# Optimization experiments

Hardware: AMD Instinct MI355X
Metric: run time of the kernel (lower is better)

Reference implementation:

```python
import jax, jax.numpy as jnp
import numpy as np

N_NODES = 50000
N_EDGES = 600000
D_IN = 128
D_OUT = 128


def setup_inputs() -> dict:
    key = jax.random.key(0)
    k1, k2, k3, k4, k5 = jax.random.split(key, 5)
    x = jax.random.normal(k1, (N_NODES, D_IN), dtype=jnp.float32)
    src = jax.random.randint(k2, (N_EDGES,), 0, N_NODES, dtype=jnp.int64)
    # guarantee every node has at least one incoming edge so in_degree >= 1
    # (DGL graphs in this repo use self-loop-augmented graphs; sqrt(deg) must be > 0)
    dst_rand = jax.random.randint(k3, (N_EDGES - N_NODES,), 0, N_NODES, dtype=jnp.int64)
    dst = jnp.concatenate([jnp.arange(N_NODES, dtype=jnp.int64), dst_rand])
    W = jax.random.normal(k4, (D_IN, D_OUT), dtype=jnp.float32) * (1.0 / np.sqrt(D_IN))
    b = jax.random.normal(k5, (D_OUT,), dtype=jnp.float32) * 0.02
    return {"x": x, "src": src, "dst": dst, "W": W, "b": b}


def reference(x, src, dst, W, b):
    # in-degrees (graph.in_degrees()): count of edges pointing at each node
    ones = jnp.ones_like(dst, dtype=jnp.float32)
    in_deg = jax.ops.segment_sum(ones, dst, num_segments=N_NODES)  # [N]
    # per-edge normalization: 1 / sqrt(deg_src * deg_dst)
    norm = jax.lax.rsqrt(in_deg[src] * in_deg[dst])  # [E]
    # gather src features, normalize, edge-wise matmul with W, add bias per edge
    msg = (x[src] * norm[:, None]) @ W + b  # [E, D_OUT]
    # sum-scatter messages to destination nodes (dgl.function.sum)
    out = jax.ops.segment_sum(msg, dst, num_segments=N_NODES)  # [N, D_OUT]
    return out
```

## Files before the change

kernel.cpp:

```cpp
#include <hip/hip_runtime.h>

#define N_NODES 50000
#define N_EDGES 600000
#define DIM 128
#define CAP 64

static __device__ __forceinline__ int idx_is32(const void* idxbuf) {
  return ((const int*)idxbuf)[1] != 0;
}
static __device__ __forceinline__ int load_idx(const void* p, int i, int is32) {
  return is32 ? ((const int*)p)[i] : (int)((const long long*)p)[i];
}
static __device__ __forceinline__ unsigned bf16_2(float a, float b) {
  unsigned ua = __float_as_uint(a), ub = __float_as_uint(b);
  ua = (ua + 0x7fffu + ((ua >> 16) & 1u)) >> 16;
  ub = (ub + 0x7fffu + ((ub >> 16) & 1u)) >> 16;
  return ua | (ub << 16);
}

__global__ void build_k(const void* __restrict__ src, const void* __restrict__ dst,
                        int* __restrict__ cursor, unsigned short* __restrict__ sorted) {
  const int half = N_EDGES / 2;
  int e0 = blockIdx.x * blockDim.x + threadIdx.x;
  if (e0 >= half) return;
  int is32 = idx_is32(dst);
#pragma unroll
  for (int h = 0; h < 2; ++h) {
    int e = e0 + h * half;
    int d = load_idx(dst, e, is32);
    int s = load_idx(src, e, is32);
    int p = atomicAdd(&cursor[d], 1);
    if (p < CAP) sorted[(d << 6) + p] = (unsigned short)s;
  }
}

__launch_bounds__(256, 3)
__global__ void ygemm_k(const float* __restrict__ x, const float4* __restrict__ W4,
                        const int* __restrict__ deg, unsigned* __restrict__ yb) {
  __shared__ float As[32 * 132];
  __shared__ float Ws[32 * 128];
  int t = threadIdx.x;
  int n0 = blockIdx.x * 128;
  int ng = t & 15, cg = t >> 4;

  float acc[8][8];
#pragma unroll
  for (int ii = 0; ii < 8; ++ii)
#pragma unroll
    for (int jj = 0; jj < 8; ++jj) acc[ii][jj] = 0.f;

  for (int s = 0; s < 4; ++s) {
    float4* Ws4 = (float4*)Ws;
#pragma unroll
    for (int i = 0; i < 4; ++i)
      Ws4[t + i * 256] = W4[s * 32 * 32 + t + i * 256];
#pragma unroll
    for (int i = 0; i < 4; ++i) {
      int idx = t + i * 256;
      int r = idx >> 3, q = idx & 7;
      int n = n0 + r;
      float4 v = make_float4(0.f, 0.f, 0.f, 0.f);
      if (n < N_NODES) v = ((const float4*)x)[n * 32 + s * 8 + q];
      As[(q * 4 + 0) * 132 + r] = v.x;
      As[(q * 4 + 1) * 132 + r] = v.y;
      As[(q * 4 + 2) * 132 + r] = v.z;
      As[(q * 4 + 3) * 132 + r] = v.w;
    }
    __syncthreads();
#pragma unroll 2
    for (int k = 0; k < 32; ++k) {
      float4 a0 = *(const float4*)&As[k * 132 + ng * 4];
      float4 a1 = *(const float4*)&As[k * 132 + 64 + ng * 4];
      float4 w0 = *(const float4*)&Ws[k * 128 + cg * 4];
      float4 w1 = *(const float4*)&Ws[k * 128 + 64 + cg * 4];
      float a[8] = {a0.x, a0.y, a0.z, a0.w, a1.x, a1.y, a1.z, a1.w};
      float w[8] = {w0.x, w0.y, w0.z, w0.w, w1.x, w1.y, w1.z, w1.w};
#pragma unroll
      for (int ii = 0; ii < 8; ++ii)
#pragma unroll
        for (int jj = 0; jj < 8; ++jj) acc[ii][jj] += a[ii] * w[jj];
    }
    __syncthreads();
  }

#pragma unroll
  for (int ii = 0; ii < 8; ++ii) {
    int n = n0 + (ii >> 2) * 64 + ng * 4 + (ii & 3);
    if (n < N_NODES) {
      float rs = rsqrtf((float)deg[n]);
      uint2 u0, u1;
      u0.x = bf16_2(acc[ii][0] * rs, acc[ii][1] * rs);
      u0.y = bf16_2(acc[ii][2] * rs, acc[ii][3] * rs);
      u1.x = bf16_2(acc[ii][4] * rs, acc[ii][5] * rs);
      u1.y = bf16_2(acc[ii][6] * rs, acc[ii][7] * rs);
      *(uint2*)&yb[(long)n * 64 + cg * 2] = u0;
      *(uint2*)&yb[(long)n * 64 + 32 + cg * 2] = u1;
    }
  }
}

__launch_bounds__(256)
__global__ void agg_k(const unsigned* __restrict__ yb,
                      const unsigned short* __restrict__ sorted,
                      const int* __restrict__ deg, const float2* __restrict__ b2,
                      float2* __restrict__ out2) {
  long gid = (long)blockIdx.x * blockDim.x + threadIdx.x;
  int d = (int)(gid >> 6);
  int lane = (int)gid & 63;
  if (d >= N_NODES) return;
  int base = d << 6;
  int dg = deg[d];
  int cnt = min(dg, CAP);
  float ax0 = 0, ax1 = 0, ax2 = 0, ax3 = 0;
  float ay0 = 0, ay1 = 0, ay2 = 0, ay3 = 0;
  int i = 0;
  for (; i + 3 < cnt; i += 4) {
    uint2 sp = *(const uint2*)&sorted[base + i];
    int s0 = sp.x & 0xffff, s1 = sp.x >> 16;
    int s2 = sp.y & 0xffff, s3 = sp.y >> 16;
    unsigned u0 = yb[s0 * 64 + lane], u1 = yb[s1 * 64 + lane];
    unsigned u2 = yb[s2 * 64 + lane], u3 = yb[s3 * 64 + lane];
    ax0 += __uint_as_float(u0 << 16);
    ay0 += __uint_as_float(u0 & 0xffff0000u);
    ax1 += __uint_as_float(u1 << 16);
    ay1 += __uint_as_float(u1 & 0xffff0000u);
    ax2 += __uint_as_float(u2 << 16);
    ay2 += __uint_as_float(u2 & 0xffff0000u);
    ax3 += __uint_as_float(u3 << 16);
    ay3 += __uint_as_float(u3 & 0xffff0000u);
  }
  for (; i < cnt; ++i) {
    int s = sorted[base + i];
    unsigned u = yb[s * 64 + lane];
    ax0 += __uint_as_float(u << 16);
    ay0 += __uint_as_float(u & 0xffff0000u);
  }
  float rd = rsqrtf((float)dg);
  float fd = (float)dg;
  float2 bv = b2[lane];
  float2 r;
  r.x = rd * ((ax0 + ax1) + (ax2 + ax3)) + fd * bv.x;
  r.y = rd * ((ay0 + ay1) + (ay2 + ay3)) + fd * bv.y;
  out2[(long)d * 64 + lane] = r;
}

__global__ void hist_k(const void* __restrict__ dst, int* __restrict__ deg) {
  int e = blockIdx.x * blockDim.x + threadIdx.x;
  if (e >= N_EDGES) return;
  atomicAdd(&deg[load_idx(dst, e, idx_is32(dst))], 1);
}
__global__ void scatter4_k(const float4* __restrict__ x4, const void* __restrict__ src,
                           const void* __restrict__ dst, const int* __restrict__ deg,
                           float* out) {
  long gid = (long)blockIdx.x * blockDim.x + threadIdx.x;
  long e = gid >> 5;
  int lane = (int)gid & 31;
  if (e >= N_EDGES) return;
  int is32 = idx_is32(dst);
  int s = load_idx(src, (int)e, is32);
  int d = load_idx(dst, (int)e, is32);
  float nrm = rsqrtf((float)deg[s] * (float)deg[d]);
  float4 v = x4[(long)s * 32 + lane];
  float* o = out + (long)d * DIM + lane * 4;
  unsafeAtomicAdd(o + 0, v.x * nrm);
  unsafeAtomicAdd(o + 1, v.y * nrm);
  unsafeAtomicAdd(o + 2, v.z * nrm);
  unsafeAtomicAdd(o + 3, v.w * nrm);
}
__launch_bounds__(256, 3)
__global__ void gemm2_k(const float* __restrict__ agg, const float4* __restrict__ W4,
                        const float* __restrict__ b, const int* __restrict__ degi,
                        float* __restrict__ out) {
  __shared__ float As[32 * 132];
  __shared__ float Ws[32 * 128];
  int t = threadIdx.x;
  int n0 = blockIdx.x * 128;
  int ng = t & 15, cg = t >> 4;
  float acc[8][8];
#pragma unroll
  for (int ii = 0; ii < 8; ++ii)
#pragma unroll
    for (int jj = 0; jj < 8; ++jj) acc[ii][jj] = 0.f;
  for (int s = 0; s < 4; ++s) {
    float4* Ws4 = (float4*)Ws;
#pragma unroll
    for (int i = 0; i < 4; ++i)
      Ws4[t + i * 256] = W4[s * 32 * 32 + t + i * 256];
#pragma unroll
    for (int i = 0; i < 4; ++i) {
      int idx = t + i * 256;
      int r = idx >> 3, q = idx & 7;
      int n = n0 + r;
      float4 v = make_float4(0.f, 0.f, 0.f, 0.f);
      if (n < N_NODES) v = ((const float4*)agg)[n * 32 + s * 8 + q];
      As[(q * 4 + 0) * 132 + r] = v.x;
      As[(q * 4 + 1) * 132 + r] = v.y;
      As[(q * 4 + 2) * 132 + r] = v.z;
      As[(q * 4 + 3) * 132 + r] = v.w;
    }
    __syncthreads();
#pragma unroll 2
    for (int k = 0; k < 32; ++k) {
      float4 a0 = *(const float4*)&As[k * 132 + ng * 4];
      float4 a1 = *(const float4*)&As[k * 132 + 64 + ng * 4];
      float4 w0 = *(const float4*)&Ws[k * 128 + cg * 4];
      float4 w1 = *(const float4*)&Ws[k * 128 + 64 + cg * 4];
      float a[8] = {a0.x, a0.y, a0.z, a0.w, a1.x, a1.y, a1.z, a1.w};
      float w[8] = {w0.x, w0.y, w0.z, w0.w, w1.x, w1.y, w1.z, w1.w};
#pragma unroll
      for (int ii = 0; ii < 8; ++ii)
#pragma unroll
        for (int jj = 0; jj < 8; ++jj) acc[ii][jj] += a[ii] * w[jj];
    }
    __syncthreads();
  }
  float4 bv0 = ((const float4*)b)[cg];
  float4 bv1 = ((const float4*)b)[16 + cg];
#pragma unroll
  for (int ii = 0; ii < 8; ++ii) {
    int n = n0 + (ii >> 2) * 64 + ng * 4 + (ii & 3);
    if (n < N_NODES) {
      float dg = (float)degi[n];
      float4 o0, o1;
      o0.x = acc[ii][0] + dg * bv0.x; o0.y = acc[ii][1] + dg * bv0.y;
      o0.z = acc[ii][2] + dg * bv0.z; o0.w = acc[ii][3] + dg * bv0.w;
      o1.x = acc[ii][4] + dg * bv1.x; o1.y = acc[ii][5] + dg * bv1.y;
      o1.z = acc[ii][6] + dg * bv1.z; o1.w = acc[ii][7] + dg * bv1.w;
      *(float4*)&out[(long)n * 128 + cg * 4] = o0;
      *(float4*)&out[(long)n * 128 + 64 + cg * 4] = o1;
    }
  }
}

static inline size_t al(size_t x) { return (x + 255) & ~(size_t)255; }

extern "C" void kernel_launch(void* const* d_in, const int* in_sizes, int n_in,
                              void* d_out, int out_size, void* d_ws, size_t ws_size,
                              hipStream_t stream) {
  const float* x = (const float*)d_in[0];
  const void* src = d_in[1];
  const void* dst = d_in[2];
  const float* W = (const float*)d_in[3];
  const float* b = (const float*)d_in[4];
  float* out = (float*)d_out;
  char* ws = (char*)d_ws;

  size_t o_sorted = al((size_t)N_NODES * 4);
  size_t o_yb = al(o_sorted + (size_t)N_NODES * CAP * 2);
  size_t need = o_yb + (size_t)N_NODES * DIM * 2;

  int* cursor = (int*)ws;
  unsigned short* sorted = (unsigned short*)(ws + o_sorted);
  unsigned* yb = (unsigned*)(ws + o_yb);

  if (ws_size >= need) {
    hipMemsetAsync(cursor, 0, (size_t)N_NODES * 4, stream);
    build_k<<<(N_EDGES / 2 + 255) / 256, 256, 0, stream>>>(src, dst, cursor, sorted);
    ygemm_k<<<(N_NODES + 127) / 128, 256, 0, stream>>>(x, (const float4*)W, cursor, yb);
    agg_k<<<(N_NODES * 64 + 255) / 256, 256, 0, stream>>>(
        yb, sorted, cursor, (const float2*)b, (float2*)out);
  } else {
    hipMemsetAsync(cursor, 0, (size_t)N_NODES * 4, stream);
    hipMemsetAsync(out, 0, (size_t)N_NODES * DIM * 4, stream);
    hist_k<<<(N_EDGES + 255) / 256, 256, 0, stream>>>(dst, cursor);
    scatter4_k<<<((long)N_EDGES * 32 + 255) / 256, 256, 0, stream>>>(
        (const float4*)x, src, dst, cursor, out);
    gemm2_k<<<(N_NODES + 127) / 128, 256, 0, stream>>>(out, (const float4*)W, b,
                                                       cursor, out);
  }
}
```

Baseline: 174.3 us.

## Fuse build, GEMM and aggregation into one cooperative persistent kernel

Replaces the memset plus three kernel launches with a single cooperative kernel that separates the cursor clear, edge bucketing, per-node GEMM and gather-aggregation phases with grid-wide syncs. The aim is to remove launch overhead and inter-kernel gaps. The aggregation loop is also unrolled to 8 gathers per iteration for more memory-level parallelism. The trade-offs are a fixed 512-block grid capped at 2 blocks per SM by launch bounds, grid.sync costs, and a fallback to the old path if the cooperative launch fails.

```diff
diff --git a/kernel.cpp b/kernel.cpp
--- a/kernel.cpp
+++ b/kernel.cpp
@@ -1,9 +1,14 @@
 #include <hip/hip_runtime.h>
+#include <hip/hip_cooperative_groups.h>
+
+namespace cg = cooperative_groups;
 
 #define N_NODES 50000
 #define N_EDGES 600000
 #define DIM 128
 #define CAP 64
+#define GRID_BLKS 512
+#define NT ((N_NODES + 127) / 128)
 
 static __device__ __forceinline__ int idx_is32(const void* idxbuf) {
   return ((const int*)idxbuf)[1] != 0;
@@ -16,6 +21,151 @@
   ua = (ua + 0x7fffu + ((ua >> 16) & 1u)) >> 16;
   ub = (ub + 0x7fffu + ((ub >> 16) & 1u)) >> 16;
   return ua | (ub << 16);
+}
+
+__global__ __launch_bounds__(256, 2) void fused_k(
+    const float* __restrict__ x, const void* __restrict__ src,
+    const void* __restrict__ dst, const float4* __restrict__ W4,
+    const float2* __restrict__ b2, int* __restrict__ cursor,
+    unsigned short* __restrict__ sorted, unsigned* __restrict__ yb,
+    float2* __restrict__ out2) {
+  cg::grid_group grid = cg::this_grid();
+  __shared__ float As[32 * 132];
+  __shared__ float Ws[32 * 128];
+  int t = threadIdx.x;
+  int bid = blockIdx.x;
+  int gtid = bid * 256 + t;
+
+  for (int i = gtid; i < N_NODES; i += GRID_BLKS * 256) cursor[i] = 0;
+  grid.sync();
+
+  {
+    int is32 = idx_is32(dst);
+    for (int e = gtid; e < N_EDGES; e += GRID_BLKS * 256) {
+      int d = load_idx(dst, e, is32);
+      int s = load_idx(src, e, is32);
+      int p = atomicAdd(&cursor[d], 1);
+      if (p < CAP) sorted[(d << 6) + p] = (unsigned short)s;
+    }
+  }
+  grid.sync();
+
+  for (int tile = bid; tile < NT; tile += GRID_BLKS) {
+    int n0 = tile * 128;
+    int ng = t & 15, cg_ = t >> 4;
+    float acc[8][8];
+#pragma unroll
+    for (int ii = 0; ii < 8; ++ii)
+#pragma unroll
+      for (int jj = 0; jj < 8; ++jj) acc[ii][jj] = 0.f;
+
+    for (int s = 0; s < 4; ++s) {
+      float4* Ws4 = (float4*)Ws;
+#pragma unroll
+      for (int i = 0; i < 4; ++i)
+        Ws4[t + i * 256] = W4[s * 32 * 32 + t + i * 256];
+#pragma unroll
+      for (int i = 0; i < 4; ++i) {
+        int idx = t + i * 256;
+        int r = idx >> 3, q = idx & 7;
+        int n = n0 + r;
+        float4 v = make_float4(0.f, 0.f, 0.f, 0.f);
+        if (n < N_NODES) v = ((const float4*)x)[n * 32 + s * 8 + q];
+        As[(q * 4 + 0) * 132 + r] = v.x;
+        As[(q * 4 + 1) * 132 + r] = v.y;
+        As[(q * 4 + 2) * 132 + r] = v.z;
+        As[(q * 4 + 3) * 132 + r] = v.w;
+      }
+      __syncthreads();
+#pragma unroll 2
+      for (int k = 0; k < 32; ++k) {
+        float4 a0 = *(const float4*)&As[k * 132 + ng * 4];
+        float4 a1 = *(const float4*)&As[k * 132 + 64 + ng * 4];
+        float4 w0 = *(const float4*)&Ws[k * 128 + cg_ * 4];
+        float4 w1 = *(const float4*)&Ws[k * 128 + 64 + cg_ * 4];
+        float a[8] = {a0.x, a0.y, a0.z, a0.w, a1.x, a1.y, a1.z, a1.w};
+        float w[8] = {w0.x, w0.y, w0.z, w0.w, w1.x, w1.y, w1.z, w1.w};
+#pragma unroll
+        for (int ii = 0; ii < 8; ++ii)
+#pragma unroll
+          for (int jj = 0; jj < 8; ++jj) acc[ii][jj] += a[ii] * w[jj];
+      }
+      __syncthreads();
+    }
+#pragma unroll
+    for (int ii = 0; ii < 8; ++ii) {
+      int n = n0 + (ii >> 2) * 64 + ng * 4 + (ii & 3);
+      if (n < N_NODES) {
+        float rs = rsqrtf((float)cursor[n]);
+        uint2 u0, u1;
+        u0.x = bf16_2(acc[ii][0] * rs, acc[ii][1] * rs);
+        u0.y = bf16_2(acc[ii][2] * rs, acc[ii][3] * rs);
+        u1.x = bf16_2(acc[ii][4] * rs, acc[ii][5] * rs);
+        u1.y = bf16_2(acc[ii][6] * rs, acc[ii][7] * rs);
+        *(uint2*)&yb[(long)n * 64 + cg_ * 2] = u0;
+        *(uint2*)&yb[(long)n * 64 + 32 + cg_ * 2] = u1;
+      }
+    }
+  }
+  grid.sync();
+
+  {
+    int lane = gtid & 63;
+    int w0 = gtid >> 6;
+    const int nwaves = GRID_BLKS * 256 / 64;
+    for (int d = w0; d < N_NODES; d += nwaves) {
+      int base = d << 6;
+      int dg = cursor[d];
+      int cnt = min(dg, CAP);
+      float ax0 = 0, ax1 = 0, ax2 = 0, ax3 = 0, ax4 = 0, ax5 = 0, ax6 = 0, ax7 = 0;
+      float ay0 = 0, ay1 = 0, ay2 = 0, ay3 = 0, ay4 = 0, ay5 = 0, ay6 = 0, ay7 = 0;
+      int i = 0;
+      for (; i + 7 < cnt; i += 8) {
+        uint4 sp = *(const uint4*)&sorted[base + i];
+        int s0 = sp.x & 0xffff, s1 = sp.x >> 16;
+        int s2 = sp.y & 0xffff, s3 = sp.y >> 16;
+        int s4 = sp.z & 0xffff, s5 = sp.z >> 16;
+        int s6 = sp.w & 0xffff, s7 = sp.w >> 16;
+        unsigned u0 = yb[s0 * 64 + lane], u1 = yb[s1 * 64 + lane];
+        unsigned u2 = yb[s2 * 64 + lane], u3 = yb[s3 * 64 + lane];
+        unsigned u4 = yb[s4 * 64 + lane], u5 = yb[s5 * 64 + lane];
+        unsigned u6 = yb[s6 * 64 + lane], u7 = yb[s7 * 64 + lane];
+        ax0 += __uint_as_float(u0 << 16); ay0 += __uint_as_float(u0 & 0xffff0000u);
+        ax1 += __uint_as_float(u1 << 16); ay1 += __uint_as_float(u1 & 0xffff0000u);
+        ax2 += __uint_as_float(u2 << 16); ay2 += __uint_as_float(u2 & 0xffff0000u);
+        ax3 += __uint_as_float(u3 << 16); ay3 += __uint_as_float(u3 & 0xffff0000u);
+        ax4 += __uint_as_float(u4 << 16); ay4 += __uint_as_float(u4 & 0xffff0000u);
+        ax5 += __uint_as_float(u5 << 16); ay5 += __uint_as_float(u5 & 0xffff0000u);
+        ax6 += __uint_as_float(u6 << 16); ay6 += __uint_as_float(u6 & 0xffff0000u);
+        ax7 += __uint_as_float(u7 << 16); ay7 += __uint_as_float(u7 & 0xffff0000u);
+      }
+      if (i + 3 < cnt) {
+        uint2 sp = *(const uint2*)&sorted[base + i];
+        int s0 = sp.x & 0xffff, s1 = sp.x >> 16;
+        int s2 = sp.y & 0xffff, s3 = sp.y >> 16;
+        unsigned u0 = yb[s0 * 64 + lane], u1 = yb[s1 * 64 + lane];
+        unsigned u2 = yb[s2 * 64 + lane], u3 = yb[s3 * 64 + lane];
+        ax0 += __uint_as_float(u0 << 16); ay0 += __uint_as_float(u0 & 0xffff0000u);
+        ax1 += __uint_as_float(u1 << 16); ay1 += __uint_as_float(u1 & 0xffff0000u);
+        ax2 += __uint_as_float(u2 << 16); ay2 += __uint_as_float(u2 & 0xffff0000u);
+        ax3 += __uint_as_float(u3 << 16); ay3 += __uint_as_float(u3 & 0xffff0000u);
+        i += 4;
+      }
+      for (; i < cnt; ++i) {
+        int s = sorted[base + i];
+        unsigned u = yb[s * 64 + lane];
+        ax0 += __uint_as_float(u << 16);
+        ay0 += __uint_as_float(u & 0xffff0000u);
+      }
+      float rd = rsqrtf((float)dg);
+      float fd = (float)dg;
+      float2 bv = b2[lane];
+      float2 r;
+      r.x = rd * (((ax0 + ax1) + (ax2 + ax3)) + ((ax4 + ax5) + (ax6 + ax7))) + fd * bv.x;
+      r.y = rd * (((ay0 + ay1) + (ay2 + ay3)) + ((ay4 + ay5) + (ay6 + ay7))) + fd * bv.y;
+      out2[(long)d * 64 + lane] = r;
+    }
+  }
 }
 
 __global__ void build_k(const void* __restrict__ src, const void* __restrict__ dst,
@@ -41,14 +191,12 @@
   __shared__ float Ws[32 * 128];
   int t = threadIdx.x;
   int n0 = blockIdx.x * 128;
-  int ng = t & 15, cg = t >> 4;
-
+  int ng = t & 15, cg_ = t >> 4;
   float acc[8][8];
 #pragma unroll
   for (int ii = 0; ii < 8; ++ii)
 #pragma unroll
     for (int jj = 0; jj < 8; ++jj) acc[ii][jj] = 0.f;
-
   for (int s = 0; s < 4; ++s) {
     float4* Ws4 = (float4*)Ws;
 #pragma unroll
@@ -71,8 +219,8 @@
     for (int k = 0; k < 32; ++k) {
       float4 a0 = *(const float4*)&As[k * 132 + ng * 4];
       float4 a1 = *(const float4*)&As[k * 132 + 64 + ng * 4];
-      float4 w0 = *(const float4*)&Ws[k * 128 + cg * 4];
-      float4 w1 = *(const float4*)&Ws[k * 128 + 64 + cg * 4];
+      float4 w0 = *(const float4*)&Ws[k * 128 + cg_ * 4];
+      float4 w1 = *(const float4*)&Ws[k * 128 + 64 + cg_ * 4];
       float a[8] = {a0.x, a0.y, a0.z, a0.w, a1.x, a1.y, a1.z, a1.w};
       float w[8] = {w0.x, w0.y, w0.z, w0.w, w1.x, w1.y, w1.z, w1.w};
 #pragma unroll
@@ -82,7 +230,6 @@
     }
     __syncthreads();
   }
-
 #pragma unroll
   for (int ii = 0; ii < 8; ++ii) {
     int n = n0 + (ii >> 2) * 64 + ng * 4 + (ii & 3);
@@ -93,8 +240,8 @@
       u0.y = bf16_2(acc[ii][2] * rs, acc[ii][3] * rs);
       u1.x = bf16_2(acc[ii][4] * rs, acc[ii][5] * rs);
       u1.y = bf16_2(acc[ii][6] * rs, acc[ii][7] * rs);
-      *(uint2*)&yb[(long)n * 64 + cg * 2] = u0;
-      *(uint2*)&yb[(long)n * 64 + 32 + cg * 2] = u1;
+      *(uint2*)&yb[(long)n * 64 + cg_ * 2] = u0;
+      *(uint2*)&yb[(long)n * 64 + 32 + cg_ * 2] = u1;
     }
   }
 }
@@ -120,14 +267,10 @@
     int s2 = sp.y & 0xffff, s3 = sp.y >> 16;
     unsigned u0 = yb[s0 * 64 + lane], u1 = yb[s1 * 64 + lane];
     unsigned u2 = yb[s2 * 64 + lane], u3 = yb[s3 * 64 + lane];
-    ax0 += __uint_as_float(u0 << 16);
-    ay0 += __uint_as_float(u0 & 0xffff0000u);
-    ax1 += __uint_as_float(u1 << 16);
-    ay1 += __uint_as_float(u1 & 0xffff0000u);
-    ax2 += __uint_as_float(u2 << 16);
-    ay2 += __uint_as_float(u2 & 0xffff0000u);
-    ax3 += __uint_as_float(u3 << 16);
-    ay3 += __uint_as_float(u3 & 0xffff0000u);
+    ax0 += __uint_as_float(u0 << 16); ay0 += __uint_as_float(u0 & 0xffff0000u);
+    ax1 += __uint_as_float(u1 << 16); ay1 += __uint_as_float(u1 & 0xffff0000u);
+    ax2 += __uint_as_float(u2 << 16); ay2 += __uint_as_float(u2 & 0xffff0000u);
+    ax3 += __uint_as_float(u3 << 16); ay3 += __uint_as_float(u3 & 0xffff0000u);
   }
   for (; i < cnt; ++i) {
     int s = sorted[base + i];
@@ -175,7 +318,7 @@
   __shared__ float Ws[32 * 128];
   int t = threadIdx.x;
   int n0 = blockIdx.x * 128;
-  int ng = t & 15, cg = t >> 4;
+  int ng = t & 15, cg_ = t >> 4;
   float acc[8][8];
 #pragma unroll
   for (int ii = 0; ii < 8; ++ii)
@@ -203,8 +346,8 @@
     for (int k = 0; k < 32; ++k) {
       float4 a0 = *(const float4*)&As[k * 132 + ng * 4];
       float4 a1 = *(const float4*)&As[k * 132 + 64 + ng * 4];
-      float4 w0 = *(const float4*)&Ws[k * 128 + cg * 4];
-      float4 w1 = *(const float4*)&Ws[k * 128 + 64 + cg * 4];
+      float4 w0 = *(const float4*)&Ws[k * 128 + cg_ * 4];
+      float4 w1 = *(const float4*)&Ws[k * 128 + 64 + cg_ * 4];
       float a[8] = {a0.x, a0.y, a0.z, a0.w, a1.x, a1.y, a1.z, a1.w};
       float w[8] = {w0.x, w0.y, w0.z, w0.w, w1.x, w1.y, w1.z, w1.w};
 #pragma unroll
@@ -214,8 +357,8 @@
     }
     __syncthreads();
   }
-  float4 bv0 = ((const float4*)b)[cg];
-  float4 bv1 = ((const float4*)b)[16 + cg];
+  float4 bv0 = ((const float4*)b)[cg_];
+  float4 bv1 = ((const float4*)b)[16 + cg_];
 #pragma unroll
   for (int ii = 0; ii < 8; ++ii) {
     int n = n0 + (ii >> 2) * 64 + ng * 4 + (ii & 3);
@@ -226,8 +369,8 @@
       o0.z = acc[ii][2] + dg * bv0.z; o0.w = acc[ii][3] + dg * bv0.w;
       o1.x = acc[ii][4] + dg * bv1.x; o1.y = acc[ii][5] + dg * bv1.y;
       o1.z = acc[ii][6] + dg * bv1.z; o1.w = acc[ii][7] + dg * bv1.w;
-      *(float4*)&out[(long)n * 128 + cg * 4] = o0;
-      *(float4*)&out[(long)n * 128 + 64 + cg * 4] = o1;
+      *(float4*)&out[(long)n * 128 + cg_ * 4] = o0;
+      *(float4*)&out[(long)n * 128 + 64 + cg_ * 4] = o1;
     }
   }
 }
@@ -254,11 +397,21 @@
   unsigned* yb = (unsigned*)(ws + o_yb);
 
   if (ws_size >= need) {
-    hipMemsetAsync(cursor, 0, (size_t)N_NODES * 4, stream);
-    build_k<<<(N_EDGES / 2 + 255) / 256, 256, 0, stream>>>(src, dst, cursor, sorted);
-    ygemm_k<<<(N_NODES + 127) / 128, 256, 0, stream>>>(x, (const float4*)W, cursor, yb);
-    agg_k<<<(N_NODES * 64 + 255) / 256, 256, 0, stream>>>(
-        yb, sorted, cursor, (const float2*)b, (float2*)out);
+    const float4* W4 = (const float4*)W;
+    const float2* b2 = (const float2*)b;
+    float2* out2 = (float2*)out;
+    void* kargs[] = {(void*)&x,      (void*)&src,  (void*)&dst,
+                     (void*)&W4,     (void*)&b2,   (void*)&cursor,
+                     (void*)&sorted, (void*)&yb,   (void*)&out2};
+    hipError_t err = hipLaunchCooperativeKernel(
+        (const void*)fused_k, dim3(GRID_BLKS), dim3(256), kargs, 0, stream);
+    if (err != hipSuccess) {
+      hipMemsetAsync(cursor, 0, (size_t)N_NODES * 4, stream);
+      build_k<<<(N_EDGES / 2 + 255) / 256, 256, 0, stream>>>(src, dst, cursor, sorted);
+      ygemm_k<<<(N_NODES + 127) / 128, 256, 0, stream>>>(x, (const float4*)W, cursor, yb);
+      agg_k<<<(N_NODES * 64 + 255) / 256, 256, 0, stream>>>(
+          yb, sorted, cursor, (const float2*)b, (float2*)out);
+    }
   } else {
     hipMemsetAsync(cursor, 0, (size_t)N_NODES * 4, stream);
     hipMemsetAsync(out, 0, (size_t)N_NODES * DIM * 4, stream);
```

New measurement: 387.4 us. +122.3%, slower.

## Fold cursor zeroing into GEMM, move src-degree norm into aggregation, widen unroll

Applied to the files above, without the earlier changes.

The GEMM now runs first and zeroes the degree cursor itself, which removes the separate memset launch. The GEMM no longer depends on degrees, so it can precede the graph build. The per-source rsqrt(deg) scaling moves from the GEMM epilogue into the aggregation kernel, which adds a gathered deg load and an rsqrt per edge. The aggregation loop is unrolled to 8 edges with more independent accumulators for extra memory-level parallelism. The cost is more random loads in agg_k and higher register use.

```diff
diff --git a/kernel.cpp b/kernel.cpp
--- a/kernel.cpp
+++ b/kernel.cpp
@@ -18,31 +18,18 @@
   return ua | (ub << 16);
 }
 
-__global__ void build_k(const void* __restrict__ src, const void* __restrict__ dst,
-                        int* __restrict__ cursor, unsigned short* __restrict__ sorted) {
-  const int half = N_EDGES / 2;
-  int e0 = blockIdx.x * blockDim.x + threadIdx.x;
-  if (e0 >= half) return;
-  int is32 = idx_is32(dst);
-#pragma unroll
-  for (int h = 0; h < 2; ++h) {
-    int e = e0 + h * half;
-    int d = load_idx(dst, e, is32);
-    int s = load_idx(src, e, is32);
-    int p = atomicAdd(&cursor[d], 1);
-    if (p < CAP) sorted[(d << 6) + p] = (unsigned short)s;
-  }
-}
-
 __launch_bounds__(256, 3)
 __global__ void ygemm_k(const float* __restrict__ x, const float4* __restrict__ W4,
-                        const int* __restrict__ deg, unsigned* __restrict__ yb) {
+                        int* __restrict__ cursor, unsigned* __restrict__ yb) {
   __shared__ float As[32 * 132];
   __shared__ float Ws[32 * 128];
   int t = threadIdx.x;
   int n0 = blockIdx.x * 128;
-  int ng = t & 15, cg = t >> 4;
-
+  {
+    int z = blockIdx.x * 256 + t;
+    if (z < N_NODES) cursor[z] = 0;
+  }
+  int ng = t & 15, cg_ = t >> 4;
   float acc[8][8];
 #pragma unroll
   for (int ii = 0; ii < 8; ++ii)
@@ -71,8 +58,8 @@
     for (int k = 0; k < 32; ++k) {
       float4 a0 = *(const float4*)&As[k * 132 + ng * 4];
       float4 a1 = *(const float4*)&As[k * 132 + 64 + ng * 4];
-      float4 w0 = *(const float4*)&Ws[k * 128 + cg * 4];
-      float4 w1 = *(const float4*)&Ws[k * 128 + 64 + cg * 4];
+      float4 w0 = *(const float4*)&Ws[k * 128 + cg_ * 4];
+      float4 w1 = *(const float4*)&Ws[k * 128 + 64 + cg_ * 4];
       float a[8] = {a0.x, a0.y, a0.z, a0.w, a1.x, a1.y, a1.z, a1.w};
       float w[8] = {w0.x, w0.y, w0.z, w0.w, w1.x, w1.y, w1.z, w1.w};
 #pragma unroll
@@ -82,20 +69,34 @@
     }
     __syncthreads();
   }
-
 #pragma unroll
   for (int ii = 0; ii < 8; ++ii) {
     int n = n0 + (ii >> 2) * 64 + ng * 4 + (ii & 3);
     if (n < N_NODES) {
-      float rs = rsqrtf((float)deg[n]);
       uint2 u0, u1;
-      u0.x = bf16_2(acc[ii][0] * rs, acc[ii][1] * rs);
-      u0.y = bf16_2(acc[ii][2] * rs, acc[ii][3] * rs);
-      u1.x = bf16_2(acc[ii][4] * rs, acc[ii][5] * rs);
-      u1.y = bf16_2(acc[ii][6] * rs, acc[ii][7] * rs);
-      *(uint2*)&yb[(long)n * 64 + cg * 2] = u0;
-      *(uint2*)&yb[(long)n * 64 + 32 + cg * 2] = u1;
-    }
+      u0.x = bf16_2(acc[ii][0], acc[ii][1]);
+      u0.y = bf16_2(acc[ii][2], acc[ii][3]);
+      u1.x = bf16_2(acc[ii][4], acc[ii][5]);
+      u1.y = bf16_2(acc[ii][6], acc[ii][7]);
+      *(uint2*)&yb[(long)n * 64 + cg_ * 2] = u0;
+      *(uint2*)&yb[(long)n * 64 + 32 + cg_ * 2] = u1;
+    }
+  }
+}
+
+__global__ void build_k(const void* __restrict__ src, const void* __restrict__ dst,
+                        int* __restrict__ cursor, unsigned short* __restrict__ sorted) {
+  const int half = N_EDGES / 2;
+  int e0 = blockIdx.x * blockDim.x + threadIdx.x;
+  if (e0 >= half) return;
+  int is32 = idx_is32(dst);
+#pragma unroll
+  for (int h = 0; h < 2; ++h) {
+    int e = e0 + h * half;
+    int d = load_idx(dst, e, is32);
+    int s = load_idx(src, e, is32);
+    int p = atomicAdd(&cursor[d], 1);
+    if (p < CAP) sorted[(d << 6) + p] = (unsigned short)s;
   }
 }
 
@@ -111,36 +112,59 @@
   int base = d << 6;
   int dg = deg[d];
   int cnt = min(dg, CAP);
-  float ax0 = 0, ax1 = 0, ax2 = 0, ax3 = 0;
-  float ay0 = 0, ay1 = 0, ay2 = 0, ay3 = 0;
+  float ax0 = 0, ax1 = 0, ax2 = 0, ax3 = 0, ax4 = 0, ax5 = 0, ax6 = 0, ax7 = 0;
+  float ay0 = 0, ay1 = 0, ay2 = 0, ay3 = 0, ay4 = 0, ay5 = 0, ay6 = 0, ay7 = 0;
   int i = 0;
-  for (; i + 3 < cnt; i += 4) {
+  for (; i + 7 < cnt; i += 8) {
+    uint4 sp = *(const uint4*)&sorted[base + i];
+    int s0 = sp.x & 0xffff, s1 = sp.x >> 16;
+    int s2 = sp.y & 0xffff, s3 = sp.y >> 16;
+    int s4 = sp.z & 0xffff, s5 = sp.z >> 16;
+    int s6 = sp.w & 0xffff, s7 = sp.w >> 16;
+    float n0 = rsqrtf((float)deg[s0]), n1 = rsqrtf((float)deg[s1]);
+    float n2 = rsqrtf((float)deg[s2]), n3 = rsqrtf((float)deg[s3]);
+    float n4 = rsqrtf((float)deg[s4]), n5 = rsqrtf((float)deg[s5]);
+    float n6 = rsqrtf((float)deg[s6]), n7 = rsqrtf((float)deg[s7]);
+    unsigned u0 = yb[s0 * 64 + lane], u1 = yb[s1 * 64 + lane];
+    unsigned u2 = yb[s2 * 64 + lane], u3 = yb[s3 * 64 + lane];
+    unsigned u4 = yb[s4 * 64 + lane], u5 = yb[s5 * 64 + lane];
+    unsigned u6 = yb[s6 * 64 + lane], u7 = yb[s7 * 64 + lane];
+    ax0 += n0 * __uint_as_float(u0 << 16); ay0 += n0 * __uint_as_float(u0 & 0xffff0000u);
+    ax1 += n1 * __uint_as_float(u1 << 16); ay1 += n1 * __uint_as_float(u1 & 0xffff0000u);
+    ax2 += n2 * __uint_as_float(u2 << 16); ay2 += n2 * __uint_as_float(u2 & 0xffff0000u);
+    ax3 += n3 * __uint_as_float(u3 << 16); ay3 += n3 * __uint_as_float(u3 & 0xffff0000u);
+    ax4 += n4 * __uint_as_float(u4 << 16); ay4 += n4 * __uint_as_float(u4 & 0xffff0000u);
+    ax5 += n5 * __uint_as_float(u5 << 16); ay5 += n5 * __uint_as_float(u5 & 0xffff0000u);
+    ax6 += n6 * __uint_as_float(u6 << 16); ay6 += n6 * __uint_as_float(u6 & 0xffff0000u);
+    ax7 += n7 * __uint_as_float(u7 << 16); ay7 += n7 * __uint_as_float(u7 & 0xffff0000u);
+  }
+  if (i + 3 < cnt) {
     uint2 sp = *(const uint2*)&sorted[base + i];
     int s0 = sp.x & 0xffff, s1 = sp.x >> 16;
     int s2 = sp.y & 0xffff, s3 = sp.y >> 16;
+    float n0 = rsqrtf((float)deg[s0]), n1 = rsqrtf((float)deg[s1]);
+    float n2 = rsqrtf((float)deg[s2]), n3 = rsqrtf((float)deg[s3]);
     unsigned u0 = yb[s0 * 64 + lane], u1 = yb[s1 * 64 + lane];
     unsigned u2 = yb[s2 * 64 + lane], u3 = yb[s3 * 64 + lane];
-    ax0 += __uint_as_float(u0 << 16);
-    ay0 += __uint_as_float(u0 & 0xffff0000u);
-    ax1 += __uint_as_float(u1 << 16);
-    ay1 += __uint_as_float(u1 & 0xffff0000u);
-    ax2 += __uint_as_float(u2 << 16);
-    ay2 += __uint_as_float(u2 & 0xffff0000u);
-    ax3 += __uint_as_float(u3 << 16);
-    ay3 += __uint_as_float(u3 & 0xffff0000u);
+    ax0 += n0 * __uint_as_float(u0 << 16); ay0 += n0 * __uint_as_float(u0 & 0xffff0000u);
+    ax1 += n1 * __uint_as_float(u1 << 16); ay1 += n1 * __uint_as_float(u1 & 0xffff0000u);
+    ax2 += n2 * __uint_as_float(u2 << 16); ay2 += n2 * __uint_as_float(u2 & 0xffff0000u);
+    ax3 += n3 * __uint_as_float(u3 << 16); ay3 += n3 * __uint_as_float(u3 & 0xffff0000u);
+    i += 4;
   }
   for (; i < cnt; ++i) {
     int s = sorted[base + i];
+    float n = rsqrtf((float)deg[s]);
     unsigned u = yb[s * 64 + lane];
-    ax0 += __uint_as_float(u << 16);
-    ay0 += __uint_as_float(u & 0xffff0000u);
+    ax0 += n * __uint_as_float(u << 16);
+    ay0 += n * __uint_as_float(u & 0xffff0000u);
   }
   float rd = rsqrtf((float)dg);
   float fd = (float)dg;
   float2 bv = b2[lane];
   float2 r;
-  r.x = rd * ((ax0 + ax1) + (ax2 + ax3)) + fd * bv.x;
-  r.y = rd * ((ay0 + ay1) + (ay2 + ay3)) + fd * bv.y;
+  r.x = rd * (((ax0 + ax1) + (ax2 + ax3)) + ((ax4 + ax5) + (ax6 + ax7))) + fd * bv.x;
+  r.y = rd * (((ay0 + ay1) + (ay2 + ay3)) + ((ay4 + ay5) + (ay6 + ay7))) + fd * bv.y;
   out2[(long)d * 64 + lane] = r;
 }
 
@@ -175,7 +199,7 @@
   __shared__ float Ws[32 * 128];
   int t = threadIdx.x;
   int n0 = blockIdx.x * 128;
-  int ng = t & 15, cg = t >> 4;
+  int ng = t & 15, cg_ = t >> 4;
   float acc[8][8];
 #pragma unroll
   for (int ii = 0; ii < 8; ++ii)
@@ -203,8 +227,8 @@
     for (int k = 0; k < 32; ++k) {
       float4 a0 = *(const float4*)&As[k * 132 + ng * 4];
       float4 a1 = *(const float4*)&As[k * 132 + 64 + ng * 4];
-      float4 w0 = *(const float4*)&Ws[k * 128 + cg * 4];
-      float4 w1 = *(const float4*)&Ws[k * 128 + 64 + cg * 4];
+      float4 w0 = *(const float4*)&Ws[k * 128 + cg_ * 4];
+      float4 w1 = *(const float4*)&Ws[k * 128 + 64 + cg_ * 4];
       float a[8] = {a0.x, a0.y, a0.z, a0.w, a1.x, a1.y, a1.z, a1.w};
       float w[8] = {w0.x, w0.y, w0.z, w0.w, w1.x, w1.y, w1.z, w1.w};
 #pragma unroll
@@ -214,8 +238,8 @@
     }
     __syncthreads();
   }
-  float4 bv0 = ((const float4*)b)[cg];
-  float4 bv1 = ((const float4*)b)[16 + cg];
+  float4 bv0 = ((const float4*)b)[cg_];
+  float4 bv1 = ((const float4*)b)[16 + cg_];
 #pragma unroll
   for (int ii = 0; ii < 8; ++ii) {
     int n = n0 + (ii >> 2) * 64 + ng * 4 + (ii & 3);
@@ -226,8 +250,8 @@
       o0.z = acc[ii][2] + dg * bv0.z; o0.w = acc[ii][3] + dg * bv0.w;
       o1.x = acc[ii][4] + dg * bv1.x; o1.y = acc[ii][5] + dg * bv1.y;
       o1.z = acc[ii][6] + dg * bv1.z; o1.w = acc[ii][7] + dg * bv1.w;
-      *(float4*)&out[(long)n * 128 + cg * 4] = o0;
-      *(float4*)&out[(long)n * 128 + 64 + cg * 4] = o1;
+      *(float4*)&out[(long)n * 128 + cg_ * 4] = o0;
+      *(float4*)&out[(long)n * 128 + 64 + cg_ * 4] = o1;
     }
   }
 }
@@ -254,9 +278,8 @@
   unsigned* yb = (unsigned*)(ws + o_yb);
 
   if (ws_size >= need) {
-    hipMemsetAsync(cursor, 0, (size_t)N_NODES * 4, stream);
+    ygemm_k<<<(N_NODES + 127) / 128, 256, 0, stream>>>(x, (const float4*)W, cursor, yb);
     build_k<<<(N_EDGES / 2 + 255) / 256, 256, 0, stream>>>(src, dst, cursor, sorted);
-    ygemm_k<<<(N_NODES + 127) / 128, 256, 0, stream>>>(x, (const float4*)W, cursor, yb);
     agg_k<<<(N_NODES * 64 + 255) / 256, 256, 0, stream>>>(
         yb, sorted, cursor, (const float2*)b, (float2*)out);
   } else {
```

Result: slower. 179.2 us (+2.8%).
